# Kernel tuning notes

Measured on AMD Instinct MI355X. Metric: run time of the kernel, lower is better.

## Reference

```python
import jax, jax.numpy as jnp
import numpy as np

N, E, D, H = 100000, 600000, 128, 8
C = D // H  # head dim = 16


def layer_norm(x, g, b, eps=1e-5):
    mu = jnp.mean(x, axis=-1, keepdims=True)
    var = jnp.mean(jnp.square(x - mu), axis=-1, keepdims=True)
    return (x - mu) * jax.lax.rsqrt(var + eps) * g + b


def setup_inputs() -> dict:
    key = jax.random.key(0)
    ks = jax.random.split(key, 20)
    s = 1.0 / np.sqrt(D)
    u = lambda k, shp: jax.random.uniform(k, shp, jnp.float32, -s, s)
    return {
        "edge_index": jax.random.randint(ks[0], (2, E), 0, N, dtype=jnp.int64),
        "node_attr": jax.random.normal(ks[1], (N, D), jnp.float32),
        "edge_attr": jax.random.normal(ks[2], (E, D), jnp.float32),
        # TransformerConv params (PyG: lin_query/key/value with bias, lin_edge no bias, lin_skip with bias)
        "Wq": u(ks[3], (D, D)), "bq": u(ks[4], (D,)),
        "Wk": u(ks[5], (D, D)), "bk": u(ks[6], (D,)),
        "Wv": u(ks[7], (D, D)), "bv": u(ks[8], (D,)),
        "We": u(ks[9], (D, D)),
        "Wskip": u(ks[10], (D, D)), "bskip": u(ks[11], (D,)),
        # FFN
        "W1": u(ks[12], (D, D)), "b1": u(ks[13], (D,)),
        "W2": u(ks[14], (D, D)), "b2": u(ks[15], (D,)),
        # LayerNorms
        "g1": jnp.ones((D,)), "be1": jnp.zeros((D,)),
        "g2": jnp.ones((D,)), "be2": jnp.zeros((D,)),
    }


def reference(edge_index, node_attr, edge_attr, Wq, bq, Wk, bk, Wv, bv, We,
              Wskip, bskip, W1, b1, W2, b2, g1, be1, g2, be2):
    src, dst = edge_index[0], edge_index[1]  # j -> i (source_to_target)
    x = node_attr
    q = (x @ Wq + bq).reshape(N, H, C)
    k = (x @ Wk + bk).reshape(N, H, C)
    v = (x @ Wv + bv).reshape(N, H, C)
    e = (edge_attr @ We).reshape(E, H, C)

    ke = k[src] + e                               # [E,H,C]
    alpha = jnp.sum(q[dst] * ke, axis=-1) / np.sqrt(C)  # [E,H]
    # scatter-softmax over edges grouped by destination node
    amax = jax.ops.segment_max(alpha, dst, num_segments=N)
    ex = jnp.exp(alpha - amax[dst])
    denom = jax.ops.segment_sum(ex, dst, num_segments=N)
    alpha = ex / (denom[dst] + 1e-16)             # [E,H]  (dropout=0 at eval)

    msg = alpha[..., None] * (v[src] + e)         # [E,H,C]
    out = jax.ops.segment_sum(msg, dst, num_segments=N).reshape(N, D)
    out = out + x @ Wskip + bskip                 # root_weight skip

    h = x + layer_norm(out, g1, be1)
    ffn = jax.nn.silu(h @ W1 + b1) @ W2 + b2
    return h + layer_norm(ffn, g2, be2)
```

## Files before the change

### kernel.cpp

```cpp
#include <hip/hip_runtime.h>
#include <hip/hip_bf16.h>

typedef __attribute__((ext_vector_type(8))) short short8;
typedef __attribute__((ext_vector_type(4))) short short4v;
typedef __attribute__((ext_vector_type(4))) float floatx4;

#define D128 128

__device__ __forceinline__ short f2bf(float f) {
    union { float f; unsigned u; } x; x.f = f;
    unsigned r = x.u + 0x7FFFu + ((x.u >> 16) & 1u);
    return (short)(r >> 16);
}
__device__ __forceinline__ float bflo(unsigned u) { return __uint_as_float(u << 16); }
__device__ __forceinline__ float bfhi(unsigned u) { return __uint_as_float(u & 0xffff0000u); }

__global__ void wprep_kernel(const float* Wq, const float* Wk, const float* Wv,
                             const float* We, const float* Ws, const float* W1,
                             const float* W2, short* wt) {
    const float* src;
    switch (blockIdx.x) {
        case 0: src = Wq; break;
        case 1: src = Wk; break;
        case 2: src = Wv; break;
        case 3: src = Ws; break;
        case 4: src = We; break;
        case 5: src = W1; break;
        default: src = W2; break;
    }
    short* dst = wt + (size_t)blockIdx.x * D128 * D128;
    for (int i = threadIdx.x; i < D128 * D128; i += blockDim.x) {
        int k = i >> 7, n = i & 127;
        dst[n * D128 + k] = f2bf(src[i]);
    }
}

__device__ __forceinline__ void load_W(const short* __restrict__ Wt, short* Bs) {
    const short8* wp = (const short8*)Wt;
    const int tid = threadIdx.x;
#pragma unroll
    for (int it = 0; it < 8; ++it) {
        int i = it * 256 + tid;
        int n = i >> 4, kg = i & 15;
        *(short8*)(&Bs[n * 136 + kg * 8]) = wp[i];
    }
    __syncthreads();
}

template <typename TA, typename TO, int SILU>
__device__ __forceinline__ void gemm_core(const TA* __restrict__ A,
                                          const float* __restrict__ bias,
                                          TO* __restrict__ out, int M,
                                          const short* Bs) {
    const int tid = threadIdx.x;
    const int wv = tid >> 6, lane = tid & 63;
    const int m = lane & 15, quad = lane >> 4;
    const int ntiles = (M + 63) >> 6;

    for (int tile = blockIdx.x; tile < ntiles; tile += gridDim.x) {
        const int row = tile * 64 + wv * 16 + m;
        const bool valid = row < M;

        short8 af[4];
        if constexpr (sizeof(TA) == 4) {
            const float* ap = (const float*)A + (size_t)row * D128;
#pragma unroll
            for (int kk = 0; kk < 4; ++kk) {
                float4 u0 = make_float4(0.f, 0.f, 0.f, 0.f), u1 = u0;
                if (valid) {
                    u0 = *(const float4*)(ap + kk * 32 + quad * 8);
                    u1 = *(const float4*)(ap + kk * 32 + quad * 8 + 4);
                }
                short8 s;
                s[0] = f2bf(u0.x); s[1] = f2bf(u0.y); s[2] = f2bf(u0.z); s[3] = f2bf(u0.w);
                s[4] = f2bf(u1.x); s[5] = f2bf(u1.y); s[6] = f2bf(u1.z); s[7] = f2bf(u1.w);
                af[kk] = s;
            }
        } else {
            const short8* ap = (const short8*)((const short*)A + (size_t)row * D128);
#pragma unroll
            for (int kk = 0; kk < 4; ++kk) {
                short8 s;
#pragma unroll
                for (int j = 0; j < 8; ++j) s[j] = 0;
                if (valid) s = ap[kk * 4 + quad];
                af[kk] = s;
            }
        }

        floatx4 acc[8];
#pragma unroll
        for (int t = 0; t < 8; ++t) acc[t] = (floatx4){0.f, 0.f, 0.f, 0.f};

#pragma unroll
        for (int kk = 0; kk < 4; ++kk) {
            const int kq = kk * 32 + quad * 8;
#pragma unroll
            for (int t = 0; t < 8; ++t) {
                short8 bf = *(const short8*)(&Bs[(t * 16 + m) * 136 + kq]);
                acc[t] = __builtin_amdgcn_mfma_f32_16x16x32_bf16(bf, af[kk], acc[t], 0, 0, 0);
            }
        }

        if (valid) {
            TO* op = out + (size_t)row * D128;
#pragma unroll
            for (int t = 0; t < 8; ++t) {
                const int c = t * 16 + quad * 4;
                float4 bv = make_float4(0.f, 0.f, 0.f, 0.f);
                if (bias) bv = *(const float4*)(bias + c);
                float v0 = acc[t][0] + bv.x;
                float v1 = acc[t][1] + bv.y;
                float v2 = acc[t][2] + bv.z;
                float v3 = acc[t][3] + bv.w;
                if (SILU) {
                    v0 = v0 / (1.f + __expf(-v0));
                    v1 = v1 / (1.f + __expf(-v1));
                    v2 = v2 / (1.f + __expf(-v2));
                    v3 = v3 / (1.f + __expf(-v3));
                }
                if constexpr (sizeof(TO) == 4) {
                    *(float4*)(op + c) = make_float4(v0, v1, v2, v3);
                } else {
                    short4v s;
                    s.x = f2bf(v0); s.y = f2bf(v1); s.z = f2bf(v2); s.w = f2bf(v3);
                    *(short4v*)(op + c) = s;
                }
            }
        }
    }
}

template <typename TA, typename TO, int SILU>
__global__ __launch_bounds__(256) void gemmP(const TA* __restrict__ A,
                                             const short* __restrict__ Wt,
                                             const float* __restrict__ bias,
                                             TO* __restrict__ out, int M) {
    __shared__ __attribute__((aligned(16))) short Bs[128 * 136];
    load_W(Wt, Bs);
    gemm_core<TA, TO, SILU>(A, bias, out, M, Bs);
}

__global__ __launch_bounds__(256) void gemm_qkvs(const float* __restrict__ x,
                                                 const short* __restrict__ wt,
                                                 const float* __restrict__ bq,
                                                 const float* __restrict__ bk,
                                                 const float* __restrict__ bv,
                                                 const float* __restrict__ bs,
                                                 short* __restrict__ q,
                                                 short* __restrict__ k,
                                                 short* __restrict__ v,
                                                 short* __restrict__ s, int M) {
    __shared__ __attribute__((aligned(16))) short Bs[128 * 136];
    const int y = blockIdx.y;
    load_W(wt + (size_t)y * 16384, Bs);
    const float* bias = (y == 0) ? bq : (y == 1) ? bk : (y == 2) ? bv : bs;
    short* out = (y == 0) ? q : (y == 1) ? k : (y == 2) ? v : s;
    gemm_core<float, short, 0>(x, bias, out, M, Bs);
}

__global__ void hist_kernel(const int* __restrict__ ei, int* __restrict__ deg, int E) {
    int i = blockIdx.x * 256 + threadIdx.x;
    if (i < E) atomicAdd(&deg[ei[(size_t)E + i]], 1);
}

__global__ __launch_bounds__(256) void scan_a(const int* __restrict__ deg,
                                              int* __restrict__ rowstart,
                                              int* __restrict__ partials, int N) {
    __shared__ int lds[256];
    int base = blockIdx.x * 1024;
    int t = threadIdx.x;
    int v[4];
    int s = 0;
#pragma unroll
    for (int j = 0; j < 4; ++j) {
        int i = base + t * 4 + j;
        v[j] = (i < N) ? deg[i] : 0;
        s += v[j];
    }
    lds[t] = s;
    __syncthreads();
    int val = s;
    for (int off = 1; off < 256; off <<= 1) {
        int other = (t >= off) ? lds[t - off] : 0;
        __syncthreads();
        val += other;
        lds[t] = val;
        __syncthreads();
    }
    int excl = val - s;
#pragma unroll
    for (int j = 0; j < 4; ++j) {
        int i = base + t * 4 + j;
        if (i < N) rowstart[i] = excl;
        excl += v[j];
    }
    if (t == 255) partials[blockIdx.x] = val;
}

__global__ __launch_bounds__(256) void scan_b(int* __restrict__ partials, int n) {
    __shared__ int lds[256];
    int t = threadIdx.x;
    int s = (t < n) ? partials[t] : 0;
    lds[t] = s;
    __syncthreads();
    int val = s;
    for (int off = 1; off < 256; off <<= 1) {
        int other = (t >= off) ? lds[t - off] : 0;
        __syncthreads();
        val += other;
        lds[t] = val;
        __syncthreads();
    }
    if (t < n) partials[t] = val - s;
}

__global__ void scan_c(int* __restrict__ rowstart, const int* __restrict__ partials,
                       int N, int Etot) {
    int i = blockIdx.x * 256 + threadIdx.x;
    if (i < N) rowstart[i] += partials[i >> 10];
    if (i == 0) rowstart[N] = Etot;
}

__global__ void fill_kernel(const int* __restrict__ ei, int* __restrict__ cursor,
                            int2* __restrict__ cst, int E) {
    int i = blockIdx.x * 256 + threadIdx.x;
    if (i >= E) return;
    int src = ei[i], dst = ei[(size_t)E + i];
    int slot = atomicAdd(&cursor[dst], 1);
    cst[slot] = make_int2(src, i);
}

__global__ __launch_bounds__(256) void attn_gather(const int* __restrict__ rowstart,
                                                   const int2* __restrict__ cst,
                                                   const unsigned* __restrict__ q2,
                                                   const unsigned* __restrict__ k2,
                                                   const unsigned* __restrict__ v2,
                                                   const unsigned* __restrict__ e2,
                                                   float* __restrict__ attn, int N) {
    int t = threadIdx.x;
    int node = blockIdx.x * 4 + (t >> 6);
    if (node >= N) return;
    int l = t & 63;
    unsigned qu = q2[(size_t)node * 64 + l];
    float q0 = bflo(qu), q1 = bfhi(qu);
    int p0 = rowstart[node], p1 = rowstart[node + 1];
    float num0 = 0.f, num1 = 0.f, den = 0.f;
    for (int p = p0; p < p1; ++p) {
        int2 se = cst[p];
        unsigned ku = k2[(size_t)se.x * 64 + l];
        unsigned eu = e2[(size_t)se.y * 64 + l];
        unsigned vu = v2[(size_t)se.x * 64 + l];
        float ke0 = bflo(ku) + bflo(eu), ke1 = bfhi(ku) + bfhi(eu);
        float pd = q0 * ke0 + q1 * ke1;
        pd += __shfl_xor(pd, 1);
        pd += __shfl_xor(pd, 2);
        pd += __shfl_xor(pd, 4);
        float ex = __expf(pd * 0.25f);
        den += ex;
        num0 += ex * (bflo(vu) + bflo(eu));
        num1 += ex * (bfhi(vu) + bfhi(eu));
    }
    float inv = 1.f / (den + 1e-16f);
    float2 o;
    o.x = num0 * inv;
    o.y = num1 * inv;
    *(float2*)(attn + (size_t)node * D128 + l * 2) = o;
}

__global__ __launch_bounds__(256) void ln_h_kernel(const float* __restrict__ attn,
                                                   const unsigned* __restrict__ skip2,
                                                   const float* __restrict__ x,
                                                   const float* __restrict__ g,
                                                   const float* __restrict__ b,
                                                   float* __restrict__ h, int N) {
    int t = threadIdx.x;
    int r = blockIdx.x * 4 + (t >> 6);
    if (r >= N) return;
    int l = t & 63;
    int c0 = l * 2;
    size_t base = (size_t)r * D128;
    float2 a = *(const float2*)(attn + base + c0);
    unsigned su = skip2[(size_t)r * 64 + l];
    float v0 = a.x + bflo(su), v1 = a.y + bfhi(su);
    float sum = v0 + v1;
#pragma unroll
    for (int o = 32; o > 0; o >>= 1) sum += __shfl_xor(sum, o);
    float mu = sum * (1.f / 128.f);
    float d0 = v0 - mu, d1 = v1 - mu;
    float vs = d0 * d0 + d1 * d1;
#pragma unroll
    for (int o = 32; o > 0; o >>= 1) vs += __shfl_xor(vs, o);
    float rs = rsqrtf(vs * (1.f / 128.f) + 1e-5f);
    float2 xe = *(const float2*)(x + base + c0);
    float2 o2;
    o2.x = xe.x + d0 * rs * g[c0] + b[c0];
    o2.y = xe.y + d1 * rs * g[c0 + 1] + b[c0 + 1];
    *(float2*)(h + base + c0) = o2;
}

__global__ __launch_bounds__(256) void ln_out_kernel(const float* __restrict__ ffn,
                                                     const float* __restrict__ h,
                                                     const float* __restrict__ g,
                                                     const float* __restrict__ b,
                                                     float* __restrict__ out, int N) {
    int t = threadIdx.x;
    int r = blockIdx.x * 4 + (t >> 6);
    if (r >= N) return;
    int c0 = (t & 63) * 2;
    size_t base = (size_t)r * D128;
    float2 f = *(const float2*)(ffn + base + c0);
    float v0 = f.x, v1 = f.y;
    float sum = v0 + v1;
#pragma unroll
    for (int o = 32; o > 0; o >>= 1) sum += __shfl_xor(sum, o);
    float mu = sum * (1.f / 128.f);
    float d0 = v0 - mu, d1 = v1 - mu;
    float vs = d0 * d0 + d1 * d1;
#pragma unroll
    for (int o = 32; o > 0; o >>= 1) vs += __shfl_xor(vs, o);
    float rs = rsqrtf(vs * (1.f / 128.f) + 1e-5f);
    float2 he = *(const float2*)(h + base + c0);
    float2 o2;
    o2.x = he.x + d0 * rs * g[c0] + b[c0];
    o2.y = he.y + d1 * rs * g[c0 + 1] + b[c0 + 1];
    *(float2*)(out + base + c0) = o2;
}

extern "C" void kernel_launch(void* const* d_in, const int* in_sizes, int n_in,
                              void* d_out, int out_size, void* d_ws, size_t ws_size,
                              hipStream_t stream) {
    const int*   ei    = (const int*)d_in[0];
    const float* x     = (const float*)d_in[1];
    const float* ea    = (const float*)d_in[2];
    const float* Wq    = (const float*)d_in[3];
    const float* bq    = (const float*)d_in[4];
    const float* Wk    = (const float*)d_in[5];
    const float* bk    = (const float*)d_in[6];
    const float* Wv    = (const float*)d_in[7];
    const float* bv    = (const float*)d_in[8];
    const float* We    = (const float*)d_in[9];
    const float* Wsk   = (const float*)d_in[10];
    const float* bskip = (const float*)d_in[11];
    const float* W1    = (const float*)d_in[12];
    const float* b1    = (const float*)d_in[13];
    const float* W2    = (const float*)d_in[14];
    const float* b2    = (const float*)d_in[15];
    const float* g1    = (const float*)d_in[16];
    const float* be1   = (const float*)d_in[17];
    const float* g2    = (const float*)d_in[18];
    const float* be2   = (const float*)d_in[19];

    const int N = in_sizes[1] / D128;
    const int E = in_sizes[2] / D128;
    const size_t nd = (size_t)N * D128;
    const size_t ed = (size_t)E * D128;

    char* p = (char*)d_ws;
    auto alloc = [&](size_t bytes) {
        char* r = p;
        p += (bytes + 255) & ~(size_t)255;
        return (void*)r;
    };
    short* qb       = (short*)alloc(nd * 2);
    short* kb       = (short*)alloc(nd * 2);
    short* vb       = (short*)alloc(nd * 2);
    short* sb       = (short*)alloc(nd * 2);
    short* ebuf     = (short*)alloc(ed * 2);
    float* attn     = (float*)alloc(nd * 4);
    float* h        = (float*)alloc(nd * 4);
    short* t1b      = (short*)alloc(nd * 2);
    float* ffn      = (float*)alloc(nd * 4);
    short* wt       = (short*)alloc(7 * 16384 * 2);
    int*   deg      = (int*)alloc((size_t)N * 4);
    int*   rowstart = (int*)alloc(((size_t)N + 1) * 4);
    int*   partials = (int*)alloc(512 * 4);
    int*   cursor   = (int*)alloc((size_t)N * 4);
    int2*  cst      = (int2*)alloc((size_t)E * 8);

    const int tilesN = (N + 63) / 64;
    const int tilesE = (E + 63) / 64;
    const int gxN = tilesN < 1024 ? tilesN : 1024;
    const int gxE = tilesE < 1024 ? tilesE : 1024;
    const int gxQ = tilesN < 512 ? tilesN : 512;
    const int nchunks = (N + 1023) / 1024;

    wprep_kernel<<<7, 256, 0, stream>>>(Wq, Wk, Wv, We, Wsk, W1, W2, wt);

    hipMemsetAsync(deg, 0, (size_t)N * 4, stream);
    hist_kernel<<<(E + 255) / 256, 256, 0, stream>>>(ei, deg, E);
    scan_a<<<nchunks, 256, 0, stream>>>(deg, rowstart, partials, N);
    scan_b<<<1, 256, 0, stream>>>(partials, nchunks);
    scan_c<<<(N + 255) / 256, 256, 0, stream>>>(rowstart, partials, N, E);
    hipMemcpyAsync(cursor, rowstart, (size_t)N * 4, hipMemcpyDeviceToDevice, stream);
    fill_kernel<<<(E + 255) / 256, 256, 0, stream>>>(ei, cursor, cst, E);

    gemm_qkvs<<<dim3(gxQ, 4), 256, 0, stream>>>(x, wt, bq, bk, bv, bskip,
                                                qb, kb, vb, sb, N);
    gemmP<float, short, 0><<<gxE, 256, 0, stream>>>(ea, wt + 4 * 16384, nullptr, ebuf, E);

    attn_gather<<<(N + 3) / 4, 256, 0, stream>>>(rowstart, cst, (const unsigned*)qb,
                                                 (const unsigned*)kb, (const unsigned*)vb,
                                                 (const unsigned*)ebuf, attn, N);

    ln_h_kernel<<<(N + 3) / 4, 256, 0, stream>>>(attn, (const unsigned*)sb, x, g1, be1, h, N);
    gemmP<float, short, 1><<<gxN, 256, 0, stream>>>(h, wt + 5 * 16384, b1, t1b, N);
    gemmP<short, float, 0><<<gxN, 256, 0, stream>>>(t1b, wt + 6 * 16384, b2, ffn, N);
    ln_out_kernel<<<(N + 3) / 4, 256, 0, stream>>>(ffn, h, g2, be2, (float*)d_out, N);
}
```

Before: 907.2 us.

## Fuse attention with LayerNorm, fuse FFN2 with LayerNorm, permute edge GEMM output

```diff
diff --git a/kernel.cpp b/kernel.cpp
--- a/kernel.cpp
+++ b/kernel.cpp
@@ -51,7 +51,8 @@
 __device__ __forceinline__ void gemm_core(const TA* __restrict__ A,
                                           const float* __restrict__ bias,
                                           TO* __restrict__ out, int M,
-                                          const short* Bs) {
+                                          const short* Bs,
+                                          const int* __restrict__ rowmap) {
     const int tid = threadIdx.x;
     const int wv = tid >> 6, lane = tid & 63;
     const int m = lane & 15, quad = lane >> 4;
@@ -103,16 +104,17 @@
         }
 
         if (valid) {
-            TO* op = out + (size_t)row * D128;
+            size_t orow = rowmap ? (size_t)rowmap[row] : (size_t)row;
+            TO* op = out + orow * D128;
 #pragma unroll
             for (int t = 0; t < 8; ++t) {
                 const int c = t * 16 + quad * 4;
-                float4 bv = make_float4(0.f, 0.f, 0.f, 0.f);
-                if (bias) bv = *(const float4*)(bias + c);
-                float v0 = acc[t][0] + bv.x;
-                float v1 = acc[t][1] + bv.y;
-                float v2 = acc[t][2] + bv.z;
-                float v3 = acc[t][3] + bv.w;
+                floatx4 bv = (floatx4){0.f, 0.f, 0.f, 0.f};
+                if (bias) bv = *(const floatx4*)(bias + c);
+                float v0 = acc[t][0] + bv[0];
+                float v1 = acc[t][1] + bv[1];
+                float v2 = acc[t][2] + bv[2];
+                float v3 = acc[t][3] + bv[3];
                 if (SILU) {
                     v0 = v0 / (1.f + __expf(-v0));
                     v1 = v1 / (1.f + __expf(-v1));
@@ -120,7 +122,7 @@
                     v3 = v3 / (1.f + __expf(-v3));
                 }
                 if constexpr (sizeof(TO) == 4) {
-                    *(float4*)(op + c) = make_float4(v0, v1, v2, v3);
+                    *(floatx4*)(op + c) = (floatx4){v0, v1, v2, v3};
                 } else {
                     short4v s;
                     s.x = f2bf(v0); s.y = f2bf(v1); s.z = f2bf(v2); s.w = f2bf(v3);
@@ -135,10 +137,11 @@
 __global__ __launch_bounds__(256) void gemmP(const TA* __restrict__ A,
                                              const short* __restrict__ Wt,
                                              const float* __restrict__ bias,
-                                             TO* __restrict__ out, int M) {
+                                             TO* __restrict__ out, int M,
+                                             const int* __restrict__ rowmap) {
     __shared__ __attribute__((aligned(16))) short Bs[128 * 136];
     load_W(Wt, Bs);
-    gemm_core<TA, TO, SILU>(A, bias, out, M, Bs);
+    gemm_core<TA, TO, SILU>(A, bias, out, M, Bs, rowmap);
 }
 
 __global__ __launch_bounds__(256) void gemm_qkvs(const float* __restrict__ x,
@@ -156,7 +159,97 @@
     load_W(wt + (size_t)y * 16384, Bs);
     const float* bias = (y == 0) ? bq : (y == 1) ? bk : (y == 2) ? bv : bs;
     short* out = (y == 0) ? q : (y == 1) ? k : (y == 2) ? v : s;
-    gemm_core<float, short, 0>(x, bias, out, M, Bs);
+    gemm_core<float, short, 0>(x, bias, out, M, Bs, nullptr);
+}
+
+__global__ __launch_bounds__(256) void gemm_ln_out(const short* __restrict__ A,
+                                                   const short* __restrict__ Wt,
+                                                   const float* __restrict__ bias,
+                                                   const float* __restrict__ h,
+                                                   const float* __restrict__ g,
+                                                   const float* __restrict__ b,
+                                                   float* __restrict__ out, int M) {
+    __shared__ __attribute__((aligned(16))) short Bs[128 * 136];
+    load_W(Wt, Bs);
+    const int tid = threadIdx.x;
+    const int wv = tid >> 6, lane = tid & 63;
+    const int m = lane & 15, quad = lane >> 4;
+    const int ntiles = (M + 63) >> 6;
+
+    for (int tile = blockIdx.x; tile < ntiles; tile += gridDim.x) {
+        const int row = tile * 64 + wv * 16 + m;
+        const bool valid = row < M;
+
+        short8 af[4];
+        const short8* ap = (const short8*)(A + (size_t)row * D128);
+#pragma unroll
+        for (int kk = 0; kk < 4; ++kk) {
+            short8 s;
+#pragma unroll
+            for (int j = 0; j < 8; ++j) s[j] = 0;
+            if (valid) s = ap[kk * 4 + quad];
+            af[kk] = s;
+        }
+
+        floatx4 acc[8];
+#pragma unroll
+        for (int t = 0; t < 8; ++t) acc[t] = (floatx4){0.f, 0.f, 0.f, 0.f};
+
+#pragma unroll
+        for (int kk = 0; kk < 4; ++kk) {
+            const int kq = kk * 32 + quad * 8;
+#pragma unroll
+            for (int t = 0; t < 8; ++t) {
+                short8 bf = *(const short8*)(&Bs[(t * 16 + m) * 136 + kq]);
+                acc[t] = __builtin_amdgcn_mfma_f32_16x16x32_bf16(bf, af[kk], acc[t], 0, 0, 0);
+            }
+        }
+
+        float vals[8][4];
+        float sum = 0.f;
+#pragma unroll
+        for (int t = 0; t < 8; ++t) {
+            const int c = t * 16 + quad * 4;
+            floatx4 bv = *(const floatx4*)(bias + c);
+#pragma unroll
+            for (int r = 0; r < 4; ++r) {
+                float v = acc[t][r] + bv[r];
+                vals[t][r] = v;
+                sum += v;
+            }
+        }
+        sum += __shfl_xor(sum, 16);
+        sum += __shfl_xor(sum, 32);
+        float mu = sum * (1.f / 128.f);
+        float vs = 0.f;
+#pragma unroll
+        for (int t = 0; t < 8; ++t)
+#pragma unroll
+            for (int r = 0; r < 4; ++r) {
+                float d = vals[t][r] - mu;
+                vals[t][r] = d;
+                vs += d * d;
+            }
+        vs += __shfl_xor(vs, 16);
+        vs += __shfl_xor(vs, 32);
+        float rs = rsqrtf(vs * (1.f / 128.f) + 1e-5f);
+
+        if (valid) {
+            const float* hp = h + (size_t)row * D128;
+            float* op = out + (size_t)row * D128;
+#pragma unroll
+            for (int t = 0; t < 8; ++t) {
+                const int c = t * 16 + quad * 4;
+                floatx4 hv = *(const floatx4*)(hp + c);
+                floatx4 gv = *(const floatx4*)(g + c);
+                floatx4 bb = *(const floatx4*)(b + c);
+                floatx4 o;
+#pragma unroll
+                for (int r = 0; r < 4; ++r) o[r] = hv[r] + vals[t][r] * rs * gv[r] + bb[r];
+                *(floatx4*)(op + c) = o;
+            }
+        }
+    }
 }
 
 __global__ void hist_kernel(const int* __restrict__ ei, int* __restrict__ deg, int E) {
@@ -216,28 +309,37 @@
 }
 
 __global__ void scan_c(int* __restrict__ rowstart, const int* __restrict__ partials,
-                       int N, int Etot) {
+                       int* __restrict__ cursor, int N, int Etot) {
     int i = blockIdx.x * 256 + threadIdx.x;
-    if (i < N) rowstart[i] += partials[i >> 10];
+    if (i < N) {
+        int v = rowstart[i] + partials[i >> 10];
+        rowstart[i] = v;
+        cursor[i] = v;
+    }
     if (i == 0) rowstart[N] = Etot;
 }
 
 __global__ void fill_kernel(const int* __restrict__ ei, int* __restrict__ cursor,
-                            int2* __restrict__ cst, int E) {
+                            int* __restrict__ csrc, int* __restrict__ pos, int E) {
     int i = blockIdx.x * 256 + threadIdx.x;
     if (i >= E) return;
     int src = ei[i], dst = ei[(size_t)E + i];
     int slot = atomicAdd(&cursor[dst], 1);
-    cst[slot] = make_int2(src, i);
-}
-
-__global__ __launch_bounds__(256) void attn_gather(const int* __restrict__ rowstart,
-                                                   const int2* __restrict__ cst,
-                                                   const unsigned* __restrict__ q2,
-                                                   const unsigned* __restrict__ k2,
-                                                   const unsigned* __restrict__ v2,
-                                                   const unsigned* __restrict__ e2,
-                                                   float* __restrict__ attn, int N) {
+    csrc[slot] = src;
+    pos[i] = slot;
+}
+
+__global__ __launch_bounds__(256) void attn_ln_h(const int* __restrict__ rowstart,
+                                                 const int* __restrict__ csrc,
+                                                 const unsigned* __restrict__ q2,
+                                                 const unsigned* __restrict__ k2,
+                                                 const unsigned* __restrict__ v2,
+                                                 const unsigned* __restrict__ ep2,
+                                                 const unsigned* __restrict__ skip2,
+                                                 const float* __restrict__ x,
+                                                 const float* __restrict__ g,
+                                                 const float* __restrict__ b,
+                                                 float* __restrict__ h, int N) {
     int t = threadIdx.x;
     int node = blockIdx.x * 4 + (t >> 6);
     if (node >= N) return;
@@ -246,13 +348,35 @@
     float q0 = bflo(qu), q1 = bfhi(qu);
     int p0 = rowstart[node], p1 = rowstart[node + 1];
     float num0 = 0.f, num1 = 0.f, den = 0.f;
-    for (int p = p0; p < p1; ++p) {
-        int2 se = cst[p];
-        unsigned ku = k2[(size_t)se.x * 64 + l];
-        unsigned eu = e2[(size_t)se.y * 64 + l];
-        unsigned vu = v2[(size_t)se.x * 64 + l];
-        float ke0 = bflo(ku) + bflo(eu), ke1 = bfhi(ku) + bfhi(eu);
-        float pd = q0 * ke0 + q1 * ke1;
+    int p = p0;
+    for (; p + 1 < p1; p += 2) {
+        int s0 = csrc[p], s1 = csrc[p + 1];
+        unsigned ku0 = k2[(size_t)s0 * 64 + l];
+        unsigned ku1 = k2[(size_t)s1 * 64 + l];
+        unsigned eu0 = ep2[(size_t)p * 64 + l];
+        unsigned eu1 = ep2[(size_t)(p + 1) * 64 + l];
+        unsigned vu0 = v2[(size_t)s0 * 64 + l];
+        unsigned vu1 = v2[(size_t)s1 * 64 + l];
+        float ka0 = bflo(ku0) + bflo(eu0), kb0 = bfhi(ku0) + bfhi(eu0);
+        float pd0 = q0 * ka0 + q1 * kb0;
+        float ka1 = bflo(ku1) + bflo(eu1), kb1 = bfhi(ku1) + bfhi(eu1);
+        float pd1 = q0 * ka1 + q1 * kb1;
+        pd0 += __shfl_xor(pd0, 1); pd1 += __shfl_xor(pd1, 1);
+        pd0 += __shfl_xor(pd0, 2); pd1 += __shfl_xor(pd1, 2);
+        pd0 += __shfl_xor(pd0, 4); pd1 += __shfl_xor(pd1, 4);
+        float ex0 = __expf(pd0 * 0.25f);
+        float ex1 = __expf(pd1 * 0.25f);
+        den += ex0 + ex1;
+        num0 += ex0 * (bflo(vu0) + bflo(eu0)) + ex1 * (bflo(vu1) + bflo(eu1));
+        num1 += ex0 * (bfhi(vu0) + bfhi(eu0)) + ex1 * (bfhi(vu1) + bfhi(eu1));
+    }
+    if (p < p1) {
+        int s0 = csrc[p];
+        unsigned ku = k2[(size_t)s0 * 64 + l];
+        unsigned eu = ep2[(size_t)p * 64 + l];
+        unsigned vu = v2[(size_t)s0 * 64 + l];
+        float ka = bflo(ku) + bflo(eu), kb = bfhi(ku) + bfhi(eu);
+        float pd = q0 * ka + q1 * kb;
         pd += __shfl_xor(pd, 1);
         pd += __shfl_xor(pd, 2);
         pd += __shfl_xor(pd, 4);
@@ -262,27 +386,10 @@
         num1 += ex * (bfhi(vu) + bfhi(eu));
     }
     float inv = 1.f / (den + 1e-16f);
-    float2 o;
-    o.x = num0 * inv;
-    o.y = num1 * inv;
-    *(float2*)(attn + (size_t)node * D128 + l * 2) = o;
-}
-
-__global__ __launch_bounds__(256) void ln_h_kernel(const float* __restrict__ attn,
-                                                   const unsigned* __restrict__ skip2,
-                                                   const float* __restrict__ x,
-                                                   const float* __restrict__ g,
-                                                   const float* __restrict__ b,
-                                                   float* __restrict__ h, int N) {
-    int t = threadIdx.x;
-    int r = blockIdx.x * 4 + (t >> 6);
-    if (r >= N) return;
-    int l = t & 63;
-    int c0 = l * 2;
-    size_t base = (size_t)r * D128;
-    float2 a = *(const float2*)(attn + base + c0);
-    unsigned su = skip2[(size_t)r * 64 + l];
-    float v0 = a.x + bflo(su), v1 = a.y + bfhi(su);
+    float v0 = num0 * inv, v1 = num1 * inv;
+
+    unsigned su = skip2[(size_t)node * 64 + l];
+    v0 += bflo(su); v1 += bfhi(su);
     float sum = v0 + v1;
 #pragma unroll
     for (int o = 32; o > 0; o >>= 1) sum += __shfl_xor(sum, o);
@@ -292,39 +399,13 @@
 #pragma unroll
     for (int o = 32; o > 0; o >>= 1) vs += __shfl_xor(vs, o);
     float rs = rsqrtf(vs * (1.f / 128.f) + 1e-5f);
+    int c0 = l * 2;
+    size_t base = (size_t)node * D128;
     float2 xe = *(const float2*)(x + base + c0);
     float2 o2;
     o2.x = xe.x + d0 * rs * g[c0] + b[c0];
     o2.y = xe.y + d1 * rs * g[c0 + 1] + b[c0 + 1];
     *(float2*)(h + base + c0) = o2;
-}
-
-__global__ __launch_bounds__(256) void ln_out_kernel(const float* __restrict__ ffn,
-                                                     const float* __restrict__ h,
-                                                     const float* __restrict__ g,
-                                                     const float* __restrict__ b,
-                                                     float* __restrict__ out, int N) {
-    int t = threadIdx.x;
-    int r = blockIdx.x * 4 + (t >> 6);
-    if (r >= N) return;
-    int c0 = (t & 63) * 2;
-    size_t base = (size_t)r * D128;
-    float2 f = *(const float2*)(ffn + base + c0);
-    float v0 = f.x, v1 = f.y;
-    float sum = v0 + v1;
-#pragma unroll
-    for (int o = 32; o > 0; o >>= 1) sum += __shfl_xor(sum, o);
-    float mu = sum * (1.f / 128.f);
-    float d0 = v0 - mu, d1 = v1 - mu;
-    float vs = d0 * d0 + d1 * d1;
-#pragma unroll
-    for (int o = 32; o > 0; o >>= 1) vs += __shfl_xor(vs, o);
-    float rs = rsqrtf(vs * (1.f / 128.f) + 1e-5f);
-    float2 he = *(const float2*)(h + base + c0);
-    float2 o2;
-    o2.x = he.x + d0 * rs * g[c0] + b[c0];
-    o2.y = he.y + d1 * rs * g[c0 + 1] + b[c0 + 1];
-    *(float2*)(out + base + c0) = o2;
 }
 
 extern "C" void kernel_launch(void* const* d_in, const int* in_sizes, int n_in,
@@ -367,16 +448,15 @@
     short* vb       = (short*)alloc(nd * 2);
     short* sb       = (short*)alloc(nd * 2);
     short* ebuf     = (short*)alloc(ed * 2);
-    float* attn     = (float*)alloc(nd * 4);
     float* h        = (float*)alloc(nd * 4);
     short* t1b      = (short*)alloc(nd * 2);
-    float* ffn      = (float*)alloc(nd * 4);
     short* wt       = (short*)alloc(7 * 16384 * 2);
     int*   deg      = (int*)alloc((size_t)N * 4);
     int*   rowstart = (int*)alloc(((size_t)N + 1) * 4);
     int*   partials = (int*)alloc(512 * 4);
     int*   cursor   = (int*)alloc((size_t)N * 4);
-    int2*  cst      = (int2*)alloc((size_t)E * 8);
+    int*   csrc     = (int*)alloc((size_t)E * 4);
+    int*   pos      = (int*)alloc((size_t)E * 4);
 
     const int tilesN = (N + 63) / 64;
     const int tilesE = (E + 63) / 64;
@@ -391,20 +471,19 @@
     hist_kernel<<<(E + 255) / 256, 256, 0, stream>>>(ei, deg, E);
     scan_a<<<nchunks, 256, 0, stream>>>(deg, rowstart, partials, N);
     scan_b<<<1, 256, 0, stream>>>(partials, nchunks);
-    scan_c<<<(N + 255) / 256, 256, 0, stream>>>(rowstart, partials, N, E);
-    hipMemcpyAsync(cursor, rowstart, (size_t)N * 4, hipMemcpyDeviceToDevice, stream);
-    fill_kernel<<<(E + 255) / 256, 256, 0, stream>>>(ei, cursor, cst, E);
+    scan_c<<<(N + 255) / 256, 256, 0, stream>>>(rowstart, partials, cursor, N, E);
+    fill_kernel<<<(E + 255) / 256, 256, 0, stream>>>(ei, cursor, csrc, pos, E);
 
     gemm_qkvs<<<dim3(gxQ, 4), 256, 0, stream>>>(x, wt, bq, bk, bv, bskip,
                                                 qb, kb, vb, sb, N);
-    gemmP<float, short, 0><<<gxE, 256, 0, stream>>>(ea, wt + 4 * 16384, nullptr, ebuf, E);
-
-    attn_gather<<<(N + 3) / 4, 256, 0, stream>>>(rowstart, cst, (const unsigned*)qb,
-                                                 (const unsigned*)kb, (const unsigned*)vb,
-                                                 (const unsigned*)ebuf, attn, N);
-
-    ln_h_kernel<<<(N + 3) / 4, 256, 0, stream>>>(attn, (const unsigned*)sb, x, g1, be1, h, N);
-    gemmP<float, short, 1><<<gxN, 256, 0, stream>>>(h, wt + 5 * 16384, b1, t1b, N);
-    gemmP<short, float, 0><<<gxN, 256, 0, stream>>>(t1b, wt + 6 * 16384, b2, ffn, N);
-    ln_out_kernel<<<(N + 3) / 4, 256, 0, stream>>>(ffn, h, g2, be2, (float*)d_out, N);
-}
+    gemmP<float, short, 0><<<gxE, 256, 0, stream>>>(ea, wt + 4 * 16384, nullptr, ebuf, E, pos);
+
+    attn_ln_h<<<(N + 3) / 4, 256, 0, stream>>>(rowstart, csrc, (const unsigned*)qb,
+                                               (const unsigned*)kb, (const unsigned*)vb,
+                                               (const unsigned*)ebuf, (const unsigned*)sb,
+                                               x, g1, be1, h, N);
+
+    gemmP<float, short, 1><<<gxN, 256, 0, stream>>>(h, wt + 5 * 16384, b1, t1b, N, nullptr);
+    gemm_ln_out<<<gxN, 256, 0, stream>>>(t1b, wt + 6 * 16384, b2, h, g2, be2,
+                                         (float*)d_out, N);
+}
```

Measured after the change: 839.0 us. 1.08x faster.
